# Performance work log

Hardware: AMD Instinct MI355X
Metric: run time of the kernel (lower is better)

The kernel has to match this reference:

```python
import jax, jax.numpy as jnp
import numpy as np

B, C, Hsp, Wsp = 16, 256, 64, 64
NUM_HEADS = 8
NORM_GROUPS = 4
EPS = 1e-5


def setup_inputs() -> dict:
    key = jax.random.key(0)
    ks = jax.random.split(key, 6)
    x = jax.random.normal(ks[0], (B, C, Hsp, Wsp), dtype=jnp.float32)
    gn_weight = jnp.ones((C,), dtype=jnp.float32)
    gn_bias = jnp.zeros((C,), dtype=jnp.float32)
    # Conv2d 1x1 kernels == dense matrices over channels
    qkv_weight = jax.random.normal(ks[1], (3 * C, C), dtype=jnp.float32) * (1.0 / np.sqrt(C))
    proj_weight = jax.random.normal(ks[2], (C, C), dtype=jnp.float32) * (1.0 / np.sqrt(C))
    proj_bias = jax.random.normal(ks[3], (C,), dtype=jnp.float32) * 0.01
    return {
        "x": x,
        "gn_weight": gn_weight,
        "gn_bias": gn_bias,
        "qkv_weight": qkv_weight,
        "proj_weight": proj_weight,
        "proj_bias": proj_bias,
    }


def reference(x, gn_weight, gn_bias, qkv_weight, proj_weight, proj_bias):
    b, c, h, w = x.shape
    hd = c // NUM_HEADS  # head dim
    n = h * w            # number of spatial tokens

    # GroupNorm over (c//G, h, w) per group, then per-channel affine
    xg = x.reshape(b, NORM_GROUPS, -1)
    mu = jnp.mean(xg, axis=-1, keepdims=True)
    var = jnp.mean(jnp.square(xg - mu), axis=-1, keepdims=True)
    xn = ((xg - mu) * jax.lax.rsqrt(var + EPS)).reshape(b, c, h, w)
    xn = xn * gn_weight[None, :, None, None] + gn_bias[None, :, None, None]

    # 1x1 conv (no bias) == channel matmul; output channel order matches torch view(b,3,H,d,h,w)
    qkv = jnp.einsum('bchw,oc->bohw', xn, qkv_weight)  # [b, 3c, h, w]
    qkv = qkv.reshape(b, 3, NUM_HEADS, hd, n)
    q, k, v = qkv[:, 0], qkv[:, 1], qkv[:, 2]          # each [b, H, d, n]

    # Linear (kernelized) attention: softmax over keys' token axis
    k = jax.nn.softmax(k, axis=-1)
    att = jnp.einsum('bhdn,bhen->bhde', k, v)          # [b, H, d, d]
    out = jnp.einsum('bhde,bhdn->bhen', att, q)        # [b, H, d, n]
    out = out.reshape(b, c, h, w)

    # Output 1x1 conv with bias
    return jnp.einsum('bchw,oc->bohw', out, proj_weight) + proj_bias[None, :, None, None]
```

## Files before the change

### kernel.cpp

```cpp
#include <hip/hip_runtime.h>
#include <hip/hip_bf16.h>


typedef __attribute__((ext_vector_type(4))) float f32x4;
typedef __attribute__((ext_vector_type(8))) short bf16x8;
typedef __attribute__((ext_vector_type(4))) short s16x4;
typedef __attribute__((ext_vector_type(8))) unsigned short u16x8;

__device__ inline float b2f(unsigned short u) {
  unsigned int x = ((unsigned int)u) << 16;
  float f; __builtin_memcpy(&f, &x, 4); return f;
}
__device__ inline unsigned short f2b(float f) {
  unsigned int x; __builtin_memcpy(&x, &f, 4);
  x += 0x7FFFu + ((x >> 16) & 1u);
  return (unsigned short)(x >> 16);
}

__global__ void __launch_bounds__(256) k_gn_partial(const float* __restrict__ x,
                                                    float* __restrict__ partials) {
  int blk = blockIdx.x;
  int grp = blk >> 4;
  int part = blk & 15;
  const float* base = x + (size_t)grp * 262144 + (size_t)part * 16384;
  int t = threadIdx.x;
  float s = 0.f, s2 = 0.f;
  for (int i = 0; i < 16; ++i) {
    f32x4 v = *(const f32x4*)(base + (size_t)(i * 256 + t) * 4);
    s  += v[0] + v[1] + v[2] + v[3];
    s2 += v[0]*v[0] + v[1]*v[1] + v[2]*v[2] + v[3]*v[3];
  }
  for (int o = 32; o > 0; o >>= 1) { s += __shfl_down(s, o); s2 += __shfl_down(s2, o); }
  __shared__ float ls[4], ls2[4];
  int w = t >> 6;
  if ((t & 63) == 0) { ls[w] = s; ls2[w] = s2; }
  __syncthreads();
  if (t == 0) {
    partials[blk * 2] = ls[0] + ls[1] + ls[2] + ls[3];
    partials[blk * 2 + 1] = ls2[0] + ls2[1] + ls2[2] + ls2[3];
  }
}

__global__ void __launch_bounds__(256) k_finalize(const float* __restrict__ partials,
                                                  float* __restrict__ stats,
                                                  const float* __restrict__ qkvw,
                                                  unsigned short* __restrict__ Wb,
                                                  unsigned short* __restrict__ WqT) {
  int bx = blockIdx.x, t = threadIdx.x;
  if (bx == 0) {
    if (t < 64) {
      float S = 0.f, S2 = 0.f;
      for (int i = 0; i < 16; ++i) { S += partials[(t * 16 + i) * 2]; S2 += partials[(t * 16 + i) * 2 + 1]; }
      float mu = S * (1.f / 262144.f);
      float var = S2 * (1.f / 262144.f) - mu * mu;
      stats[t * 2] = mu;
      stats[t * 2 + 1] = rsqrtf(var + 1e-5f);
    }
  } else if (bx <= 192) {
    int idx = (bx - 1) * 256 + t;
    f32x4 v = *(const f32x4*)(qkvw + (size_t)idx * 4);
    s16x4 o;
    for (int i = 0; i < 4; ++i) o[i] = (short)f2b(v[i]);
    *(s16x4*)(Wb + (size_t)idx * 4) = o;
  } else {
    int bb = bx - 193;
    int c = bb * 16 + (t & 15);
    int d0 = (t >> 4) * 16;
    for (int i = 0; i < 16; ++i) {
      int d = d0 + i;
      WqT[(size_t)c * 256 + d] = f2b(qkvw[(size_t)d * 256 + c]);
    }
  }
}

__global__ void __launch_bounds__(256) k_norm_t(const float* __restrict__ x,
                                                const float* __restrict__ stats,
                                                const float* __restrict__ gamma,
                                                const float* __restrict__ beta,
                                                unsigned short* __restrict__ xnT) {
  int blk = blockIdx.x;
  int b = blk >> 8;
  int tile = blk & 255;
  int ct = tile >> 6;
  int nt = tile & 63;
  int c0 = ct * 64, n0 = nt * 64;
  __shared__ float T[64][65];
  int t = threadIdx.x;
  float mu = stats[(b * 4 + ct) * 2];
  float rs = stats[(b * 4 + ct) * 2 + 1];
  int cl = t >> 2, q4 = t & 3;
  float sc = gamma[c0 + cl] * rs;
  float off = beta[c0 + cl] - mu * sc;
  const float* xr = x + ((size_t)b * 256 + c0 + cl) * 4096 + n0;
  for (int p = 0; p < 4; ++p) {
    int col = p * 16 + q4 * 4;
    f32x4 v = *(const f32x4*)(xr + col);
    for (int i = 0; i < 4; ++i) T[cl][col + i] = v[i] * sc + off;
  }
  __syncthreads();
  int nl = t >> 2, cc = t & 3;
  u16x8 o0, o1;
  for (int i = 0; i < 8; ++i) o0[i] = f2b(T[cc * 16 + i][nl]);
  for (int i = 0; i < 8; ++i) o1[i] = f2b(T[cc * 16 + 8 + i][nl]);
  unsigned short* dst = xnT + ((size_t)b * 4096 + n0 + nl) * 256 + c0 + cc * 16;
  *(u16x8*)dst = o0;
  *(u16x8*)(dst + 8) = o1;
}

__global__ void __launch_bounds__(256, 2) k_attfused(const unsigned short* __restrict__ Wb,
                                                     const unsigned short* __restrict__ xnT,
                                                     float* __restrict__ attg,
                                                     float* __restrict__ rsums) {
  const int bx = blockIdx.x;
  const int b = bx >> 2, ns = bx & 3, h = blockIdx.y;
  const int hb = b * 8 + h;
  const int t = threadIdx.x;
  const int wave = t >> 6, lane = t & 63;
  const int g = lane >> 4, r = lane & 15;
  const int rh = wave >> 1;
  const int ch = wave & 1;
  __shared__ unsigned short PL[2][32][72];
  __shared__ unsigned short VL[2][32][72];

  const unsigned short* Wrow = Wb + (size_t)(256 + rh * 256 + h * 32) * 256;
  bf16x8 af[2][8];
#pragma unroll
  for (int rt = 0; rt < 2; ++rt)
#pragma unroll
    for (int kt = 0; kt < 8; ++kt)
      af[rt][kt] = *(const bf16x8*)(Wrow + (size_t)(rt * 16 + r) * 256 + kt * 32 + 8 * g);

  const unsigned short* Xb = xnT + ((size_t)b * 4096 + ns * 1024 + ch * 32 + r) * 256 + 8 * g;
  f32x4 attacc = {0.f, 0.f, 0.f, 0.f};
  float rs[2][4] = {{0.f,0.f,0.f,0.f},{0.f,0.f,0.f,0.f}};

  bf16x8 bfr[8][2];
#pragma unroll
  for (int kt = 0; kt < 8; ++kt) {
    bfr[kt][0] = *(const bf16x8*)(Xb + kt * 32);
    bfr[kt][1] = *(const bf16x8*)(Xb + (size_t)(16 * 256) + kt * 32);
  }

  for (int c = 0; c < 16; ++c) {
    const int cur = c & 1;
    const unsigned short* Xn = Xb + (size_t)(((c + 1) & 15) * 64) * 256;
    f32x4 sacc[2][2] = {};
    __builtin_amdgcn_s_setprio(1);
#pragma unroll
    for (int kt = 0; kt < 8; ++kt) {
      bf16x8 b0 = bfr[kt][0], b1 = bfr[kt][1];
      bfr[kt][0] = *(const bf16x8*)(Xn + kt * 32);
      bfr[kt][1] = *(const bf16x8*)(Xn + (size_t)(16 * 256) + kt * 32);
      sacc[0][0] = __builtin_amdgcn_mfma_f32_16x16x32_bf16(af[0][kt], b0, sacc[0][0], 0, 0, 0);
      sacc[0][1] = __builtin_amdgcn_mfma_f32_16x16x32_bf16(af[0][kt], b1, sacc[0][1], 0, 0, 0);
      sacc[1][0] = __builtin_amdgcn_mfma_f32_16x16x32_bf16(af[1][kt], b0, sacc[1][0], 0, 0, 0);
      sacc[1][1] = __builtin_amdgcn_mfma_f32_16x16x32_bf16(af[1][kt], b1, sacc[1][1], 0, 0, 0);
    }
    __builtin_amdgcn_s_setprio(0);
    if (rh == 0) {
#pragma unroll
      for (int rt = 0; rt < 2; ++rt)
#pragma unroll
        for (int ct = 0; ct < 2; ++ct)
#pragma unroll
          for (int reg = 0; reg < 4; ++reg) {
            float e = __expf(sacc[rt][ct][reg]);
            rs[rt][reg] += e;
            PL[cur][rt * 16 + 4 * g + reg][ch * 32 + ct * 16 + r] = f2b(e);
          }
    } else {
#pragma unroll
      for (int rt = 0; rt < 2; ++rt)
#pragma unroll
        for (int ct = 0; ct < 2; ++ct)
#pragma unroll
          for (int reg = 0; reg < 4; ++reg)
            VL[cur][rt * 16 + 4 * g + reg][ch * 32 + ct * 16 + r] = f2b(sacc[rt][ct][reg]);
    }
    __syncthreads();
#pragma unroll
    for (int ks = 0; ks < 2; ++ks) {
      bf16x8 pa = *(const bf16x8*)&PL[cur][rh * 16 + r][ks * 32 + 8 * g];
      bf16x8 vb = *(const bf16x8*)&VL[cur][ch * 16 + r][ks * 32 + 8 * g];
      attacc = __builtin_amdgcn_mfma_f32_16x16x32_bf16(pa, vb, attacc, 0, 0, 0);
    }
  }
  float* ab = attg + (size_t)hb * 1024;
#pragma unroll
  for (int reg = 0; reg < 4; ++reg)
    atomicAdd(&ab[(rh * 16 + 4 * g + reg) * 32 + ch * 16 + r], attacc[reg]);
  if (rh == 0) {
#pragma unroll
    for (int rt = 0; rt < 2; ++rt)
#pragma unroll
      for (int reg = 0; reg < 4; ++reg) {
        float v = rs[rt][reg];
        v += __shfl_xor(v, 1); v += __shfl_xor(v, 2);
        v += __shfl_xor(v, 4); v += __shfl_xor(v, 8);
        if (r == 0) atomicAdd(&rsums[hb * 32 + rt * 16 + 4 * g + reg], v);
      }
  }
}

template<bool OUT_BF16, bool ADD_BIAS>
__global__ void __launch_bounds__(256)
k_gemm_bt(const unsigned short* __restrict__ A,
          const unsigned short* __restrict__ B,
          void* __restrict__ Cv,
          const float* __restrict__ bias,
          long sA, long sB, long sC, int ldc) {
  __shared__ unsigned short LA[128][32];
  __shared__ unsigned short LB[128][32];
  const int t = threadIdx.x;
  const unsigned short* Ab = A + (size_t)blockIdx.z * sA + (size_t)blockIdx.x * 128 * 256;
  const unsigned short* Bb = B + (size_t)blockIdx.z * sB + (size_t)blockIdx.y * 128 * 256;
  const int wave = t >> 6, lane = t & 63;
  const int wm = wave >> 1, wn = wave & 1;
  const int g = lane >> 4, r = lane & 15;
  const int rA = t >> 2, sslot = t & 3;
  const int ws0 = 8 * (sslot ^ (rA & 3));
  const int rslot = 8 * (g ^ (r & 3));
  const unsigned short* ag = Ab + (size_t)rA * 256 + 8 * sslot;
  const unsigned short* bg = Bb + (size_t)rA * 256 + 8 * sslot;
  u16x8 pa0 = *(const u16x8*)(ag);
  u16x8 pa1 = *(const u16x8*)(ag + 64 * 256);
  u16x8 pb0 = *(const u16x8*)(bg);
  u16x8 pb1 = *(const u16x8*)(bg + 64 * 256);
  f32x4 acc[4][4] = {};
  for (int kt = 0; kt < 8; ++kt) {
    if (kt) __syncthreads();
    *(u16x8*)&LA[rA][ws0] = pa0;  *(u16x8*)&LA[rA + 64][ws0] = pa1;
    *(u16x8*)&LB[rA][ws0] = pb0;  *(u16x8*)&LB[rA + 64][ws0] = pb1;
    __syncthreads();
    if (kt < 7) {
      int off = (kt + 1) * 32;
      pa0 = *(const u16x8*)(ag + off);  pa1 = *(const u16x8*)(ag + 64 * 256 + off);
      pb0 = *(const u16x8*)(bg + off);  pb1 = *(const u16x8*)(bg + 64 * 256 + off);
    }
    bf16x8 af[4], bfr[4];
    for (int i = 0; i < 4; ++i) {
      af[i]  = *(const bf16x8*)&LA[wm * 64 + i * 16 + r][rslot];
      bfr[i] = *(const bf16x8*)&LB[wn * 64 + i * 16 + r][rslot];
    }
    for (int mi = 0; mi < 4; ++mi)
      for (int ni = 0; ni < 4; ++ni)
        acc[mi][ni] = __builtin_amdgcn_mfma_f32_16x16x32_bf16(af[mi], bfr[ni], acc[mi][ni], 0, 0, 0);
  }
  const int m0 = blockIdx.x * 128 + wm * 64;
  const int n0 = blockIdx.y * 128 + wn * 64;
  if (OUT_BF16) {
    unsigned short* C = (unsigned short*)Cv + (size_t)blockIdx.z * sC;
    for (int mi = 0; mi < 4; ++mi)
      for (int ni = 0; ni < 4; ++ni) {
        int row = m0 + mi * 16 + 4 * g;
        int col = n0 + ni * 16 + r;
        for (int reg = 0; reg < 4; ++reg)
          C[(size_t)(row + reg) * ldc + col] = f2b(acc[mi][ni][reg]);
      }
  } else {
    float* C = (float*)Cv + (size_t)blockIdx.z * sC;
    for (int mi = 0; mi < 4; ++mi)
      for (int ni = 0; ni < 4; ++ni) {
        int row = m0 + mi * 16 + 4 * g;
        int col = n0 + ni * 16 + r;
        for (int reg = 0; reg < 4; ++reg) {
          float v = acc[mi][ni][reg];
          if (ADD_BIAS) v += bias[row + reg];
          C[(size_t)(row + reg) * ldc + col] = v;
        }
      }
  }
}

__global__ void __launch_bounds__(256) k_makeM(const float* __restrict__ attg,
                                               const float* __restrict__ rsums,
                                               const float* __restrict__ projw,
                                               unsigned short* __restrict__ Mb) {
  int blk = blockIdx.x;
  int b = blk >> 3, h = blk & 7;
  __shared__ float attL[32][33];
  __shared__ float invs[32];
  int t = threadIdx.x;
  if (t < 32) invs[t] = 1.f / rsums[blk * 32 + t];
  const float* asrc = attg + (size_t)blk * 1024;
  {
    f32x4 v = *(const f32x4*)(asrc + (size_t)t * 4);
    int idx = t * 4;
    for (int i = 0; i < 4; ++i) attL[(idx + i) >> 5][(idx + i) & 31] = v[i];
  }
  __syncthreads();
  float pw[32];
  const float* ps = projw + (size_t)t * 256 + h * 32;
  for (int i = 0; i < 8; ++i) {
    f32x4 v = *(const f32x4*)(ps + i * 4);
    pw[i * 4 + 0] = v[0]; pw[i * 4 + 1] = v[1]; pw[i * 4 + 2] = v[2]; pw[i * 4 + 3] = v[3];
  }
  unsigned short* dst = Mb + ((size_t)b * 256 + t) * 256 + h * 32;
  for (int dd = 0; dd < 32; ++dd) {
    float s = 0.f;
    for (int e = 0; e < 32; ++e) s += pw[e] * attL[dd][e];
    dst[dd] = f2b(s * invs[dd]);
  }
}

__global__ void __launch_bounds__(256) k_gemm_final(const unsigned short* __restrict__ M2,
                                                    const unsigned short* __restrict__ xnT,
                                                    float* __restrict__ out,
                                                    const float* __restrict__ bias) {
  const int nt = blockIdx.x, b = blockIdx.y;
  const unsigned short* Ab = M2 + (size_t)b * 65536;
  const unsigned short* Bb = xnT + ((size_t)b * 4096 + nt * 64) * 256;
  float* Cb = out + (size_t)b * 1048576 + (size_t)nt * 64;
  __shared__ unsigned short LB[2][64][32];
  const int t = threadIdx.x;
  const int wave = t >> 6, lane = t & 63, g = lane >> 4, r = lane & 15;
  const int srow = t >> 2, sslot = t & 3;
  const int ws0 = 8 * (sslot ^ (srow & 3));
  const int rslot = 8 * (g ^ (r & 3));
  const unsigned short* bg = Bb + (size_t)srow * 256 + 8 * sslot;
  const unsigned short* ar = Ab + (size_t)(wave * 64 + r) * 256 + 8 * g;
  u16x8 pb = *(const u16x8*)bg;
  f32x4 acc[4][4] = {};
  for (int kt = 0; kt < 8; ++kt) {
    const int cur = kt & 1;
    *(u16x8*)&LB[cur][srow][ws0] = pb;
    __syncthreads();
    if (kt < 7) pb = *(const u16x8*)(bg + (kt + 1) * 32);
    bf16x8 af[4], bfr[4];
#pragma unroll
    for (int mi = 0; mi < 4; ++mi)
      af[mi] = *(const bf16x8*)(ar + (size_t)(mi * 16) * 256 + kt * 32);
#pragma unroll
    for (int ni = 0; ni < 4; ++ni)
      bfr[ni] = *(const bf16x8*)&LB[cur][ni * 16 + r][rslot];
#pragma unroll
    for (int mi = 0; mi < 4; ++mi)
#pragma unroll
      for (int ni = 0; ni < 4; ++ni)
        acc[mi][ni] = __builtin_amdgcn_mfma_f32_16x16x32_bf16(af[mi], bfr[ni], acc[mi][ni], 0, 0, 0);
  }
#pragma unroll
  for (int mi = 0; mi < 4; ++mi) {
    const int row = wave * 64 + mi * 16 + 4 * g;
#pragma unroll
    for (int ni = 0; ni < 4; ++ni)
#pragma unroll
      for (int reg = 0; reg < 4; ++reg)
        Cb[(size_t)(row + reg) * 4096 + ni * 16 + r] = acc[mi][ni][reg] + bias[row + reg];
  }
}

extern "C" void kernel_launch(void* const* d_in, const int* in_sizes, int n_in,
                              void* d_out, int out_size, void* d_ws, size_t ws_size,
                              hipStream_t stream) {
  (void)in_sizes; (void)n_in; (void)out_size; (void)ws_size;
  const float* x     = (const float*)d_in[0];
  const float* gn_w  = (const float*)d_in[1];
  const float* gn_b  = (const float*)d_in[2];
  const float* qkvw  = (const float*)d_in[3];
  const float* projw = (const float*)d_in[4];
  const float* projb = (const float*)d_in[5];

  char* ws = (char*)d_ws;
  float*          partials = (float*)(ws);
  float*          stats    = (float*)(ws + 8192);
  unsigned short* Wb       = (unsigned short*)(ws + 16384);
  unsigned short* Mb       = (unsigned short*)(ws + 409600);
  float*          attg     = (float*)(ws + 2506752);
  float*          rsums    = (float*)(ws + 3031040);
  unsigned short* WqT      = (unsigned short*)(ws + 3047424);
  unsigned short* M2       = (unsigned short*)(ws + 3178496);
  unsigned short* xnT      = (unsigned short*)(ws + 8388608);

  k_gn_partial<<<1024, 256, 0, stream>>>(x, partials);
  k_finalize<<<209, 256, 0, stream>>>(partials, stats, qkvw, Wb, WqT);
  k_norm_t<<<4096, 256, 0, stream>>>(x, stats, gn_w, gn_b, xnT);
  (void)hipMemsetAsync(attg, 0, 540672, stream);
  k_attfused<<<dim3(64, 8), 256, 0, stream>>>(Wb, xnT, attg, rsums);
  k_makeM<<<128, 256, 0, stream>>>(attg, rsums, projw, Mb);
  k_gemm_bt<true, false><<<dim3(2, 2, 16), 256, 0, stream>>>(
      Mb, WqT, (void*)M2, nullptr, 65536L, 0L, 65536L, 256);
  k_gemm_final<<<dim3(64, 16), 256, 0, stream>>>(M2, xnT, (float*)d_out, projb);
}
```

Measured before the change: 240.0 us.

## Stage xnT tiles into swizzled LDS via direct global-to-LDS loads

Each 64-token xnT tile is now copied into a 32KB XL shared buffer with global_load_lds, using an XOR swizzle. All four waves then read their B fragments from LDS, so waves that share the same columns no longer issue duplicate global reads. The next tile's load is started after a barrier, once the current fragments are in registers. This adds 32KB of LDS and an extra barrier per chunk, which may limit occupancy at 2 blocks per CU and exposes load latency because only one buffer is used.

```diff
diff --git a/kernel.cpp b/kernel.cpp
--- a/kernel.cpp
+++ b/kernel.cpp
@@ -119,6 +119,7 @@
   const int g = lane >> 4, r = lane & 15;
   const int rh = wave >> 1;
   const int ch = wave & 1;
+  __shared__ unsigned short XL[64][256];
   __shared__ unsigned short PL[2][32][72];
   __shared__ unsigned short VL[2][32][72];
 
@@ -130,31 +131,47 @@
     for (int kt = 0; kt < 8; ++kt)
       af[rt][kt] = *(const bf16x8*)(Wrow + (size_t)(rt * 16 + r) * 256 + kt * 32 + 8 * g);
 
-  const unsigned short* Xb = xnT + ((size_t)b * 4096 + ns * 1024 + ch * 32 + r) * 256 + 8 * g;
+  const unsigned short* slice = xnT + ((size_t)b * 4096 + ns * 1024) * 256;
+  const int swz = t >> 5;
+  const unsigned short* gstage = slice + (size_t)swz * 256 + ((t & 31) ^ swz) * 8;
+  char* lstage = (char*)&XL[0][0] + ((t >> 6) << 10);
+#pragma unroll
+  for (int i = 0; i < 8; ++i)
+    __builtin_amdgcn_global_load_lds((const void*)(gstage + (size_t)(i * 8) * 256),
+                                     (void*)(lstage + i * 4096), 16, 0, 0);
+
   f32x4 attacc = {0.f, 0.f, 0.f, 0.f};
   float rs[2][4] = {{0.f,0.f,0.f,0.f},{0.f,0.f,0.f,0.f}};
-
-  bf16x8 bfr[8][2];
-#pragma unroll
-  for (int kt = 0; kt < 8; ++kt) {
-    bfr[kt][0] = *(const bf16x8*)(Xb + kt * 32);
-    bfr[kt][1] = *(const bf16x8*)(Xb + (size_t)(16 * 256) + kt * 32);
-  }
+  const char* xl0 = (const char*)&XL[0][0];
+  __syncthreads();
 
   for (int c = 0; c < 16; ++c) {
     const int cur = c & 1;
-    const unsigned short* Xn = Xb + (size_t)(((c + 1) & 15) * 64) * 256;
+    bf16x8 bfr[8][2];
+#pragma unroll
+    for (int kt = 0; kt < 8; ++kt)
+#pragma unroll
+      for (int ct = 0; ct < 2; ++ct) {
+        const int row = ch * 32 + ct * 16 + r;
+        const int slot = (kt * 4 + g) ^ (r & 7);
+        bfr[kt][ct] = *(const bf16x8*)(xl0 + row * 512 + slot * 16);
+      }
+    __syncthreads();
+    if (c < 15) {
+      const unsigned short* gs = gstage + (size_t)(c + 1) * 64 * 256;
+#pragma unroll
+      for (int i = 0; i < 8; ++i)
+        __builtin_amdgcn_global_load_lds((const void*)(gs + (size_t)(i * 8) * 256),
+                                         (void*)(lstage + i * 4096), 16, 0, 0);
+    }
     f32x4 sacc[2][2] = {};
     __builtin_amdgcn_s_setprio(1);
 #pragma unroll
     for (int kt = 0; kt < 8; ++kt) {
-      bf16x8 b0 = bfr[kt][0], b1 = bfr[kt][1];
-      bfr[kt][0] = *(const bf16x8*)(Xn + kt * 32);
-      bfr[kt][1] = *(const bf16x8*)(Xn + (size_t)(16 * 256) + kt * 32);
-      sacc[0][0] = __builtin_amdgcn_mfma_f32_16x16x32_bf16(af[0][kt], b0, sacc[0][0], 0, 0, 0);
-      sacc[0][1] = __builtin_amdgcn_mfma_f32_16x16x32_bf16(af[0][kt], b1, sacc[0][1], 0, 0, 0);
-      sacc[1][0] = __builtin_amdgcn_mfma_f32_16x16x32_bf16(af[1][kt], b0, sacc[1][0], 0, 0, 0);
-      sacc[1][1] = __builtin_amdgcn_mfma_f32_16x16x32_bf16(af[1][kt], b1, sacc[1][1], 0, 0, 0);
+      sacc[0][0] = __builtin_amdgcn_mfma_f32_16x16x32_bf16(af[0][kt], bfr[kt][0], sacc[0][0], 0, 0, 0);
+      sacc[0][1] = __builtin_amdgcn_mfma_f32_16x16x32_bf16(af[0][kt], bfr[kt][1], sacc[0][1], 0, 0, 0);
+      sacc[1][0] = __builtin_amdgcn_mfma_f32_16x16x32_bf16(af[1][kt], bfr[kt][0], sacc[1][0], 0, 0, 0);
+      sacc[1][1] = __builtin_amdgcn_mfma_f32_16x16x32_bf16(af[1][kt], bfr[kt][1], sacc[1][1], 0, 0, 0);
     }
     __builtin_amdgcn_s_setprio(0);
     if (rh == 0) {
```

Measured after the change: 205.7 us. 1.17x faster.
